# Kernel optimization log

Hardware: AMD Instinct MI355X
Metric: run time of the kernel (lower is better)

Reference implementation:

```python
import jax, jax.numpy as jnp
import numpy as np

DIM = 384
HEADS = 6
DIM_HEAD = 64
INNER = HEADS * DIM_HEAD  # 384


def setup_inputs() -> dict:
    key = jax.random.key(0)
    ks = jax.random.split(key, 6)
    s = 0.02
    return {
        "x_q": jax.random.normal(ks[0], (8, 4096, DIM), dtype=jnp.float32),
        "x_kv": jax.random.normal(ks[1], (8, 4096, DIM), dtype=jnp.float32),
        "Wq": jax.random.normal(ks[2], (DIM, INNER), dtype=jnp.float32) * s,
        "Wkv": jax.random.normal(ks[3], (DIM, 2 * INNER), dtype=jnp.float32) * s,
        "Wout": jax.random.normal(ks[4], (INNER, DIM), dtype=jnp.float32) * s,
        "bout": jax.random.normal(ks[5], (DIM,), dtype=jnp.float32) * s,
    }


def _split_heads(t, b, n):
    # [b, n, h*d] -> [b, h, n, d]
    return t.reshape(b, n, HEADS, DIM_HEAD).transpose(0, 2, 1, 3)


def reference(x_q, x_kv, Wq, Wkv, Wout, bout):
    b, nq, _ = x_q.shape
    nkv = x_kv.shape[1]
    q = x_q @ Wq                      # [b, nq, inner]
    kv_proj = x_kv @ Wkv              # [b, nkv, 2*inner]
    k, v = jnp.split(kv_proj, 2, axis=-1)
    q = _split_heads(q, b, nq)        # [b, h, nq, d]
    k = _split_heads(k, b, nkv)       # [b, h, nkv, d]
    v = _split_heads(v, b, nkv)       # [b, h, nkv, d]
    q = jax.nn.elu(q) + 1.0
    k = jax.nn.elu(k) + 1.0
    kv = jnp.einsum('bhnd,bhnm->bhdm', k, v)             # [b, h, d, d]
    z = 1.0 / (jnp.einsum('bhnd,bhd->bhn', q, k.sum(axis=2)) + 1e-6)
    out = jnp.einsum('bhnd,bhdm->bhnm', q, kv) * z[..., None]  # [b, h, nq, d]
    out = out.transpose(0, 2, 1, 3).reshape(b, nq, INNER)
    return out @ Wout + bout
```

## Files before the change

kernel.cpp:

```cpp
#include <hip/hip_runtime.h>
#include <math.h>

#define BATCH 8
#define SEQ 4096
#define DIMSZ 384
#define HEADS 6
#define DH 64
#define MTOT (BATCH * SEQ)
#define KD 384

typedef short short8 __attribute__((ext_vector_type(8)));
typedef float floatx4 __attribute__((ext_vector_type(4)));
typedef unsigned short ushort4v __attribute__((ext_vector_type(4)));
typedef unsigned short ushort8v __attribute__((ext_vector_type(8)));
typedef unsigned int uint2v __attribute__((ext_vector_type(2)));
typedef unsigned int uint4v __attribute__((ext_vector_type(4)));

__device__ __forceinline__ float elu1(float x) { return x > 0.f ? x + 1.f : __expf(x); }

__device__ __forceinline__ unsigned short f2b(float f) {
    unsigned int u = __float_as_uint(f);
    u = (u + 0x7fffu + ((u >> 16) & 1u)) >> 16;
    return (unsigned short)u;
}
__device__ __forceinline__ float b2f(unsigned short u) {
    return __uint_as_float(((unsigned int)u) << 16);
}
__device__ __forceinline__ unsigned int f2b2(float lo, float hi) {
    unsigned int r;
    asm("v_cvt_pk_bf16_f32 %0, %1, %2" : "=v"(r) : "v"(lo), "v"(hi));
    return r;
}

__device__ __forceinline__ void gl16(const void* g, void* l) {
    __builtin_amdgcn_global_load_lds((const __attribute__((address_space(1))) unsigned int*)g,
                                     (__attribute__((address_space(3))) unsigned int*)l, 16, 0, 0);
}

__global__ __launch_bounds__(256) void conv_wt3(const float* __restrict__ Wq,
                                                const float* __restrict__ Wkv,
                                                const float* __restrict__ Wout,
                                                unsigned short* __restrict__ WqT,
                                                unsigned short* __restrict__ WkvT,
                                                unsigned short* __restrict__ WoutT) {
    __shared__ float tile[32][33];
    int bx = blockIdx.x;
    const float* W;
    unsigned short* WT;
    int N;
    if (bx < 12) { W = Wq; WT = WqT; N = DIMSZ; }
    else if (bx < 36) { W = Wkv; WT = WkvT; N = 2 * DIMSZ; bx -= 12; }
    else { W = Wout; WT = WoutT; N = DIMSZ; bx -= 36; }
    const int n0 = bx * 32, k0 = blockIdx.y * 32;
    const int tx = threadIdx.x & 31, ty = threadIdx.x >> 5;
#pragma unroll
    for (int i = 0; i < 32; i += 8) tile[ty + i][tx] = W[(size_t)(k0 + ty + i) * N + n0 + tx];
    __syncthreads();
#pragma unroll
    for (int i = 0; i < 32; i += 8)
        WT[(size_t)(n0 + ty + i) * KD + k0 + tx] = f2b(tile[tx][ty + i]);
}

__global__ __launch_bounds__(256, 4) void gemm_kv(const float* __restrict__ A,
                                                  const unsigned short* __restrict__ WkvT,
                                                  float* __restrict__ pkv,
                                                  float* __restrict__ pks) {
    __shared__ __align__(16) unsigned short buf[17408];
    __shared__ float ksLDS[128];
    unsigned short* As = buf;
    unsigned short* Bs = buf + 8192;
    const int tid = threadIdx.x;
    const int lane = tid & 63, wave = tid >> 6;
    const int l15 = lane & 15, qd = lane >> 4;
    const int fid = blockIdx.x;
    const int xcd = fid & 7;
    const int s = fid >> 3;
    const int h = s % HEADS;
    const int rtl = s / HEADS;
    const int row0 = (xcd * 32 + rtl) * 128;
    const int pidx = (xcd * HEADS + h) * 32 + rtl;
    const int wm = (wave & 1) * 64, wn = (wave >> 1) * 64;

    const float* Ab = A + (size_t)row0 * KD;
    const unsigned short* Bb = WkvT + (size_t)(h * DH) * KD;
    const int srow = tid >> 3;
    const int scol = (((tid & 7) ^ (srow & 7)) * 8);

    floatx4 zero = {0.f, 0.f, 0.f, 0.f};
    floatx4 acc[4][4];
#pragma unroll
    for (int i = 0; i < 4; ++i)
#pragma unroll
        for (int j = 0; j < 4; ++j) acc[i][j] = zero;

    const int sw = l15 & 7;
    for (int kk = 0; kk < KD; kk += 64) {
        __syncthreads();
#pragma unroll
        for (int i = 0; i < 4; ++i)
            gl16(Bb + (size_t)(i * 32 + srow + (i >= 2 ? 320 : 0)) * KD + kk + scol,
                 Bs + i * 2048 + wave * 512);
        float4 g0[4], g1[4];
#pragma unroll
        for (int i = 0; i < 4; ++i) {
            const float* src = Ab + (size_t)(i * 32 + srow) * KD + kk + scol;
            g0[i] = *(const float4*)src;
            g1[i] = *(const float4*)(src + 4);
        }
#pragma unroll
        for (int i = 0; i < 4; ++i) {
            uint4v u;
            u[0] = f2b2(g0[i].x, g0[i].y);
            u[1] = f2b2(g0[i].z, g0[i].w);
            u[2] = f2b2(g1[i].x, g1[i].y);
            u[3] = f2b2(g1[i].z, g1[i].w);
            *(uint4v*)&As[i * 2048 + tid * 8] = u;
        }
        __syncthreads();
#pragma unroll
        for (int t = 0; t < 2; ++t) {
            const int chnk = ((t * 4 + qd) ^ sw) * 8;
            short8 af[4], bfr[4];
#pragma unroll
            for (int mi = 0; mi < 4; ++mi)
                af[mi] = *(const short8*)&As[(wm + mi * 16 + l15) * 64 + chnk];
#pragma unroll
            for (int ni = 0; ni < 4; ++ni)
                bfr[ni] = *(const short8*)&Bs[(wn + ni * 16 + l15) * 64 + chnk];
#pragma unroll
            for (int mi = 0; mi < 4; ++mi)
#pragma unroll
                for (int ni = 0; ni < 4; ++ni)
                    acc[mi][ni] = __builtin_amdgcn_mfma_f32_16x16x32_bf16(af[mi], bfr[ni],
                                                                          acc[mi][ni], 0, 0, 0);
        }
    }

    __syncthreads();
    const bool kw = (wn == 0);
    float ksp[4] = {};
#pragma unroll
    for (int mi = 0; mi < 4; ++mi)
#pragma unroll
        for (int ni = 0; ni < 4; ++ni) {
            const int rb = wm + mi * 16 + qd * 4;
            const int cl = wn + ni * 16 + l15;
            float v0 = acc[mi][ni][0], v1 = acc[mi][ni][1];
            float v2 = acc[mi][ni][2], v3 = acc[mi][ni][3];
            if (kw) {
                v0 = elu1(v0); v1 = elu1(v1); v2 = elu1(v2); v3 = elu1(v3);
                ksp[ni] += (v0 + v1) + (v2 + v3);
            }
            uint2v o;
            o[0] = f2b2(v0, v1);
            o[1] = f2b2(v2, v3);
            *(uint2v*)&buf[cl * 136 + rb] = o;
        }
    if (kw) {
#pragma unroll
        for (int ni = 0; ni < 4; ++ni) {
            float v = ksp[ni];
            v += __shfl_xor(v, 16);
            v += __shfl_xor(v, 32);
            if (lane < 16) ksLDS[wave * 64 + ni * 16 + lane] = v;
        }
    }
    __syncthreads();
    floatx4 kva[4];
#pragma unroll
    for (int j = 0; j < 4; ++j) kva[j] = zero;
#pragma unroll
    for (int nk = 0; nk < 4; ++nk) {
        short8 afk = *(const short8*)&buf[(wave * 16 + l15) * 136 + nk * 32 + qd * 8];
#pragma unroll
        for (int nj = 0; nj < 4; ++nj) {
            short8 bfv = *(const short8*)&buf[(64 + nj * 16 + l15) * 136 + nk * 32 + qd * 8];
            kva[nj] = __builtin_amdgcn_mfma_f32_16x16x32_bf16(afk, bfv, kva[nj], 0, 0, 0);
        }
    }
    float* P = pkv + (size_t)pidx * 4096;
#pragma unroll
    for (int nj = 0; nj < 4; ++nj)
#pragma unroll
        for (int r = 0; r < 4; ++r)
            P[(wave * 16 + qd * 4 + r) * 64 + nj * 16 + l15] = kva[nj][r];
    if (tid < 64) pks[pidx * 64 + tid] = ksLDS[tid] + ksLDS[64 + tid];
}

__global__ __launch_bounds__(256) void kv_reduce(const float* __restrict__ pkv,
                                                 const float* __restrict__ pks,
                                                 unsigned short* __restrict__ kv_bf,
                                                 float* __restrict__ ksum_g) {
    const int bh = blockIdx.x >> 2, dc = blockIdx.x & 3;
    const int tid = threadIdx.x;
    unsigned short* kb = kv_bf + (size_t)bh * 4096;
    const int i0 = dc * 1024 + tid * 4;
    float4 sum = {0.f, 0.f, 0.f, 0.f};
#pragma unroll
    for (int c = 0; c < 32; ++c) {
        float4 p = *(const float4*)&pkv[(size_t)(bh * 32 + c) * 4096 + i0];
        sum.x += p.x; sum.y += p.y; sum.z += p.z; sum.w += p.w;
    }
    const int d = i0 >> 6, m = i0 & 63;
    kb[(m + 0) * 64 + d] = f2b(sum.x);
    kb[(m + 1) * 64 + d] = f2b(sum.y);
    kb[(m + 2) * 64 + d] = f2b(sum.z);
    kb[(m + 3) * 64 + d] = f2b(sum.w);
    if (dc == 0 && tid < 64) {
        float s = 0.f;
#pragma unroll
        for (int c = 0; c < 32; ++c) s += pks[(bh * 32 + c) * 64 + tid];
        ksum_g[bh * 64 + tid] = s;
    }
}

__global__ __launch_bounds__(256, 3) void gemm_q_attn(const float* __restrict__ A,
                                                      const unsigned short* __restrict__ WqT,
                                                      const unsigned short* __restrict__ kv_bf,
                                                      const float* __restrict__ ksum_g,
                                                      unsigned short* __restrict__ attn) {
    __shared__ __align__(16) unsigned short buf[17408];
    __shared__ float ksh[128];
    __shared__ float zsh[256];
    unsigned short* As = buf;
    unsigned short* Bs = buf + 8192;
    const int tid = threadIdx.x;
    const int lane = tid & 63, wave = tid >> 6;
    const int l15 = lane & 15, qd = lane >> 4;
    const int fid = blockIdx.x;
    const int xcd = fid & 7;
    const int s = fid >> 3;
    const int ct = s % 3;
    const int rtl = s / 3;
    const int row0 = (xcd * 32 + rtl) * 128;
    const int col0 = ct * 128;
    const int bh0 = xcd * HEADS + ct * 2;
    const int wd = (wave & 1) * 64, wn2 = (wave >> 1) * 64;

    if (tid < 128) ksh[tid] = ksum_g[bh0 * 64 + tid];

    const float* Ab = A + (size_t)row0 * KD;
    const unsigned short* Bb = WqT + (size_t)col0 * KD;
    const int srow = tid >> 3;
    const int scol = (((tid & 7) ^ (srow & 7)) * 8);

    floatx4 zero = {0.f, 0.f, 0.f, 0.f};
    floatx4 acc[4][4];
#pragma unroll
    for (int i = 0; i < 4; ++i)
#pragma unroll
        for (int j = 0; j < 4; ++j) acc[i][j] = zero;

    const int sw = l15 & 7;
    for (int kk = 0; kk < KD; kk += 64) {
        __syncthreads();
#pragma unroll
        for (int i = 0; i < 4; ++i)
            gl16(Bb + (size_t)(i * 32 + srow) * KD + kk + scol, Bs + i * 2048 + wave * 512);
        float4 g0[4], g1[4];
#pragma unroll
        for (int i = 0; i < 4; ++i) {
            const float* src = Ab + (size_t)(i * 32 + srow) * KD + kk + scol;
            g0[i] = *(const float4*)src;
            g1[i] = *(const float4*)(src + 4);
        }
#pragma unroll
        for (int i = 0; i < 4; ++i) {
            uint4v u;
            u[0] = f2b2(g0[i].x, g0[i].y);
            u[1] = f2b2(g0[i].z, g0[i].w);
            u[2] = f2b2(g1[i].x, g1[i].y);
            u[3] = f2b2(g1[i].z, g1[i].w);
            *(uint4v*)&As[i * 2048 + tid * 8] = u;
        }
        __syncthreads();
#pragma unroll
        for (int t = 0; t < 2; ++t) {
            const int chnk = ((t * 4 + qd) ^ sw) * 8;
            short8 wf[4], xf[4];
#pragma unroll
            for (int di = 0; di < 4; ++di)
                wf[di] = *(const short8*)&Bs[(wd + di * 16 + l15) * 64 + chnk];
#pragma unroll
            for (int nj = 0; nj < 4; ++nj)
                xf[nj] = *(const short8*)&As[(wn2 + nj * 16 + l15) * 64 + chnk];
#pragma unroll
            for (int di = 0; di < 4; ++di)
#pragma unroll
                for (int nj = 0; nj < 4; ++nj)
                    acc[di][nj] = __builtin_amdgcn_mfma_f32_16x16x32_bf16(wf[di], xf[nj],
                                                                          acc[di][nj], 0, 0, 0);
        }
    }

    float zp[4] = {};
#pragma unroll
    for (int di = 0; di < 4; ++di)
#pragma unroll
        for (int r = 0; r < 4; ++r) {
            const float ks = ksh[wd + di * 16 + qd * 4 + r];
#pragma unroll
            for (int nj = 0; nj < 4; ++nj) {
                const float q = elu1(acc[di][nj][r]);
                acc[di][nj][r] = q;
                zp[nj] += q * ks;
            }
        }
#pragma unroll
    for (int nj = 0; nj < 4; ++nj) {
        float v = zp[nj];
        v += __shfl_xor(v, 16);
        v += __shfl_xor(v, 32);
        zp[nj] = 1.f / (v + 1e-6f);
    }
    __syncthreads();
    if (lane < 16) {
#pragma unroll
        for (int nj = 0; nj < 4; ++nj) zsh[(wave & 1) * 128 + wn2 + nj * 16 + lane] = zp[nj];
    }
#pragma unroll
    for (int di = 0; di < 4; ++di)
#pragma unroll
        for (int nj = 0; nj < 4; ++nj) {
            const int rb = wd + di * 16 + qd * 4;
            const int cl = wn2 + nj * 16 + l15;
            uint2v o;
            o[0] = f2b2(acc[di][nj][0], acc[di][nj][1]);
            o[1] = f2b2(acc[di][nj][2], acc[di][nj][3]);
            *(uint2v*)&buf[cl * 136 + rb] = o;
        }
    __syncthreads();
    const int hh = wave & 1;
    const unsigned short* kvB = kv_bf + (size_t)(bh0 + hh) * 4096;
    floatx4 acc2[4][4];
#pragma unroll
    for (int i = 0; i < 4; ++i)
#pragma unroll
        for (int j = 0; j < 4; ++j) acc2[i][j] = zero;
#pragma unroll
    for (int t = 0; t < 2; ++t) {
        short8 bf2[4];
#pragma unroll
        for (int bj = 0; bj < 4; ++bj)
            bf2[bj] = *(const short8*)&kvB[(bj * 16 + l15) * 64 + t * 32 + qd * 8];
#pragma unroll
        for (int ai = 0; ai < 4; ++ai) {
            short8 af =
                *(const short8*)&buf[(wn2 + ai * 16 + l15) * 136 + hh * 64 + t * 32 + qd * 8];
#pragma unroll
            for (int bj = 0; bj < 4; ++bj)
                acc2[ai][bj] =
                    __builtin_amdgcn_mfma_f32_16x16x32_bf16(af, bf2[bj], acc2[ai][bj], 0, 0, 0);
        }
    }
#pragma unroll
    for (int ai = 0; ai < 4; ++ai)
#pragma unroll
        for (int bj = 0; bj < 4; ++bj) {
            const int colg = col0 + hh * 64 + bj * 16 + l15;
#pragma unroll
            for (int r = 0; r < 4; ++r) {
                const int nl = wn2 + ai * 16 + qd * 4 + r;
                const float v = acc2[ai][bj][r] * zsh[hh * 128 + nl];
                attn[(size_t)(row0 + nl) * KD + colg] = f2b(v);
            }
        }
}

__global__ __launch_bounds__(256, 4) void gemm_out(const unsigned short* __restrict__ A,
                                                   const unsigned short* __restrict__ BT,
                                                   float* __restrict__ C,
                                                   const float* __restrict__ bias) {
    __shared__ __align__(16) unsigned short buf[17408];
    unsigned short* As = buf;
    unsigned short* Bs = buf + 8192;
    const int tid = threadIdx.x;
    const int lane = tid & 63, wave = tid >> 6;
    const int l15 = lane & 15, qd = lane >> 4;
    const int fid = blockIdx.x;
    const int xcd = fid & 7;
    const int s = fid >> 3;
    const int row0 = (xcd * 32 + s / 3) * 128;
    const int col0 = (s % 3) * 128;
    const int wm = (wave & 1) * 64, wn = (wave >> 1) * 64;

    const unsigned short* Ab = A + (size_t)row0 * KD;
    const unsigned short* Bb = BT + (size_t)col0 * KD;
    const int srow = tid >> 3;
    const int scol = (((tid & 7) ^ (srow & 7)) * 8);

    floatx4 zero = {0.f, 0.f, 0.f, 0.f};
    floatx4 acc[4][4];
#pragma unroll
    for (int i = 0; i < 4; ++i)
#pragma unroll
        for (int j = 0; j < 4; ++j) acc[i][j] = zero;

    const int sw = l15 & 7;
    for (int kk = 0; kk < KD; kk += 64) {
        __syncthreads();
#pragma unroll
        for (int i = 0; i < 4; ++i)
            gl16(Ab + (size_t)(i * 32 + srow) * KD + kk + scol, As + i * 2048 + wave * 512);
#pragma unroll
        for (int i = 0; i < 4; ++i)
            gl16(Bb + (size_t)(i * 32 + srow) * KD + kk + scol, Bs + i * 2048 + wave * 512);
        __syncthreads();
#pragma unroll
        for (int t = 0; t < 2; ++t) {
            const int chnk = ((t * 4 + qd) ^ sw) * 8;
            short8 af[4], bfr[4];
#pragma unroll
            for (int mi = 0; mi < 4; ++mi)
                af[mi] = *(const short8*)&As[(wm + mi * 16 + l15) * 64 + chnk];
#pragma unroll
            for (int ni = 0; ni < 4; ++ni)
                bfr[ni] = *(const short8*)&Bs[(wn + ni * 16 + l15) * 64 + chnk];
#pragma unroll
            for (int mi = 0; mi < 4; ++mi)
#pragma unroll
                for (int ni = 0; ni < 4; ++ni)
                    acc[mi][ni] = __builtin_amdgcn_mfma_f32_16x16x32_bf16(af[mi], bfr[ni],
                                                                          acc[mi][ni], 0, 0, 0);
        }
    }
#pragma unroll
    for (int mi = 0; mi < 4; ++mi)
#pragma unroll
        for (int ni = 0; ni < 4; ++ni) {
            const int rbase = row0 + wm + mi * 16 + qd * 4;
            const int col = col0 + wn + ni * 16 + l15;
            const float bsv = bias[col];
#pragma unroll
            for (int r = 0; r < 4; ++r)
                __builtin_nontemporal_store(acc[mi][ni][r] + bsv,
                                            &C[(size_t)(rbase + r) * DIMSZ + col]);
        }
}

extern "C" void kernel_launch(void* const* d_in, const int* in_sizes, int n_in,
                              void* d_out, int out_size, void* d_ws, size_t ws_size,
                              hipStream_t stream) {
    const float* x_q = (const float*)d_in[0];
    const float* x_kv = (const float*)d_in[1];
    const float* Wq = (const float*)d_in[2];
    const float* Wkv = (const float*)d_in[3];
    const float* Wout = (const float*)d_in[4];
    const float* bout = (const float*)d_in[5];
    float* out = (float*)d_out;

    char* ws = (char*)d_ws;
    float* pkv = (float*)(ws + 0);
    unsigned short* attn_bf = (unsigned short*)(ws + 0);
    unsigned short* WqT = (unsigned short*)(ws + 25165824);
    unsigned short* WkvT = (unsigned short*)(ws + 25460736);
    unsigned short* WoutT = (unsigned short*)(ws + 26050560);
    float* ksum = (float*)(ws + 26345472);
    float* pks = (float*)(ws + 26357760);
    unsigned short* kv_bf = (unsigned short*)(ws + 26750976);

    dim3 blk(256);
    conv_wt3<<<dim3(48, 12), blk, 0, stream>>>(Wq, Wkv, Wout, WqT, WkvT, WoutT);
    gemm_kv<<<dim3(1536), blk, 0, stream>>>(x_kv, WkvT, pkv, pks);
    kv_reduce<<<dim3(192), blk, 0, stream>>>(pkv, pks, kv_bf, ksum);
    gemm_q_attn<<<dim3(768), blk, 0, stream>>>(x_q, WqT, kv_bf, ksum, attn_bf);
    gemm_out<<<dim3(768), blk, 0, stream>>>(attn_bf, WoutT, out, bout);
}
```

Before: 218.2 us.

## Register-prefetch next A tile across barriers in all three GEMM kernels

In each of the three GEMM main loops, the next k-slice of the A operand is loaded into registers before the barrier. The barrier is replaced with a custom s_waitcnt that only waits for the older LDS-direct B loads and leaves the prefetch outstanding. Global latency for A therefore overlaps with the MFMA work on the current tile. The cost is more live registers, so gemm_kv's launch bound drops to 3 waves, which risks lower occupancy. Correctness depends on the hand-counted vmcnt values matching the order the compiler emits the loads in.

```diff
diff --git a/kernel.cpp b/kernel.cpp
--- a/kernel.cpp
+++ b/kernel.cpp
@@ -36,6 +36,25 @@
     __builtin_amdgcn_global_load_lds((const __attribute__((address_space(1))) unsigned int*)g,
                                      (__attribute__((address_space(3))) unsigned int*)l, 16, 0, 0);
 }
+
+#define BARRIER_EXEMPT8()                                              \
+    do {                                                               \
+        asm volatile("s_waitcnt vmcnt(8) lgkmcnt(0)" ::: "memory");    \
+        __builtin_amdgcn_s_barrier();                                  \
+        __builtin_amdgcn_sched_barrier(0);                             \
+    } while (0)
+#define BARRIER_EXEMPT4()                                              \
+    do {                                                               \
+        asm volatile("s_waitcnt vmcnt(4) lgkmcnt(0)" ::: "memory");    \
+        __builtin_amdgcn_s_barrier();                                  \
+        __builtin_amdgcn_sched_barrier(0);                             \
+    } while (0)
+#define BARRIER_DRAIN()                                                \
+    do {                                                               \
+        asm volatile("s_waitcnt vmcnt(0) lgkmcnt(0)" ::: "memory");    \
+        __builtin_amdgcn_s_barrier();                                  \
+        __builtin_amdgcn_sched_barrier(0);                             \
+    } while (0)
 
 __global__ __launch_bounds__(256) void conv_wt3(const float* __restrict__ Wq,
                                                 const float* __restrict__ Wkv,
@@ -61,7 +80,7 @@
         WT[(size_t)(n0 + ty + i) * KD + k0 + tx] = f2b(tile[tx][ty + i]);
 }
 
-__global__ __launch_bounds__(256, 4) void gemm_kv(const float* __restrict__ A,
+__global__ __launch_bounds__(256, 3) void gemm_kv(const float* __restrict__ A,
                                                   const unsigned short* __restrict__ WkvT,
                                                   float* __restrict__ pkv,
                                                   float* __restrict__ pks) {
@@ -94,19 +113,20 @@
         for (int j = 0; j < 4; ++j) acc[i][j] = zero;
 
     const int sw = l15 & 7;
+    float4 g0[4], g1[4];
+#pragma unroll
+    for (int i = 0; i < 4; ++i) {
+        const float* src = Ab + (size_t)(i * 32 + srow) * KD + scol;
+        g0[i] = *(const float4*)src;
+        g1[i] = *(const float4*)(src + 4);
+    }
+#pragma unroll
     for (int kk = 0; kk < KD; kk += 64) {
         __syncthreads();
 #pragma unroll
         for (int i = 0; i < 4; ++i)
             gl16(Bb + (size_t)(i * 32 + srow + (i >= 2 ? 320 : 0)) * KD + kk + scol,
                  Bs + i * 2048 + wave * 512);
-        float4 g0[4], g1[4];
-#pragma unroll
-        for (int i = 0; i < 4; ++i) {
-            const float* src = Ab + (size_t)(i * 32 + srow) * KD + kk + scol;
-            g0[i] = *(const float4*)src;
-            g1[i] = *(const float4*)(src + 4);
-        }
 #pragma unroll
         for (int i = 0; i < 4; ++i) {
             uint4v u;
@@ -116,7 +136,17 @@
             u[3] = f2b2(g1[i].z, g1[i].w);
             *(uint4v*)&As[i * 2048 + tid * 8] = u;
         }
-        __syncthreads();
+        if (kk + 64 < KD) {
+#pragma unroll
+            for (int i = 0; i < 4; ++i) {
+                const float* src = Ab + (size_t)(i * 32 + srow) * KD + kk + 64 + scol;
+                g0[i] = *(const float4*)src;
+                g1[i] = *(const float4*)(src + 4);
+            }
+            BARRIER_EXEMPT8();
+        } else {
+            BARRIER_DRAIN();
+        }
 #pragma unroll
         for (int t = 0; t < 2; ++t) {
             const int chnk = ((t * 4 + qd) ^ sw) * 8;
@@ -252,18 +282,19 @@
         for (int j = 0; j < 4; ++j) acc[i][j] = zero;
 
     const int sw = l15 & 7;
+    float4 g0[4], g1[4];
+#pragma unroll
+    for (int i = 0; i < 4; ++i) {
+        const float* src = Ab + (size_t)(i * 32 + srow) * KD + scol;
+        g0[i] = *(const float4*)src;
+        g1[i] = *(const float4*)(src + 4);
+    }
+#pragma unroll
     for (int kk = 0; kk < KD; kk += 64) {
         __syncthreads();
 #pragma unroll
         for (int i = 0; i < 4; ++i)
             gl16(Bb + (size_t)(i * 32 + srow) * KD + kk + scol, Bs + i * 2048 + wave * 512);
-        float4 g0[4], g1[4];
-#pragma unroll
-        for (int i = 0; i < 4; ++i) {
-            const float* src = Ab + (size_t)(i * 32 + srow) * KD + kk + scol;
-            g0[i] = *(const float4*)src;
-            g1[i] = *(const float4*)(src + 4);
-        }
 #pragma unroll
         for (int i = 0; i < 4; ++i) {
             uint4v u;
@@ -273,7 +304,17 @@
             u[3] = f2b2(g1[i].z, g1[i].w);
             *(uint4v*)&As[i * 2048 + tid * 8] = u;
         }
-        __syncthreads();
+        if (kk + 64 < KD) {
+#pragma unroll
+            for (int i = 0; i < 4; ++i) {
+                const float* src = Ab + (size_t)(i * 32 + srow) * KD + kk + 64 + scol;
+                g0[i] = *(const float4*)src;
+                g1[i] = *(const float4*)(src + 4);
+            }
+            BARRIER_EXEMPT8();
+        } else {
+            BARRIER_DRAIN();
+        }
 #pragma unroll
         for (int t = 0; t < 2; ++t) {
             const int chnk = ((t * 4 + qd) ^ sw) * 8;
@@ -397,15 +438,27 @@
         for (int j = 0; j < 4; ++j) acc[i][j] = zero;
 
     const int sw = l15 & 7;
+    ushort8v ga[4];
+#pragma unroll
+    for (int i = 0; i < 4; ++i)
+        ga[i] = *(const ushort8v*)(Ab + (size_t)(i * 32 + srow) * KD + scol);
+#pragma unroll
     for (int kk = 0; kk < KD; kk += 64) {
         __syncthreads();
 #pragma unroll
         for (int i = 0; i < 4; ++i)
-            gl16(Ab + (size_t)(i * 32 + srow) * KD + kk + scol, As + i * 2048 + wave * 512);
+            gl16(Bb + (size_t)(i * 32 + srow) * KD + kk + scol, Bs + i * 2048 + wave * 512);
 #pragma unroll
         for (int i = 0; i < 4; ++i)
-            gl16(Bb + (size_t)(i * 32 + srow) * KD + kk + scol, Bs + i * 2048 + wave * 512);
-        __syncthreads();
+            *(ushort8v*)&As[i * 2048 + tid * 8] = ga[i];
+        if (kk + 64 < KD) {
+#pragma unroll
+            for (int i = 0; i < 4; ++i)
+                ga[i] = *(const ushort8v*)(Ab + (size_t)(i * 32 + srow) * KD + kk + 64 + scol);
+            BARRIER_EXEMPT4();
+        } else {
+            BARRIER_DRAIN();
+        }
 #pragma unroll
         for (int t = 0; t < 2; ++t) {
             const int chnk = ((t * 4 + qd) ^ sw) * 8;
```

Result: slower. 227.9 us (+4.4%).
